# Performance work log

Hardware: AMD Instinct MI355X
Metric: run time of the kernel (lower is better)

Reference implementation:

```python
import jax, jax.numpy as jnp
import numpy as np

WIN = (8, 7, 7)
SHIFT = (4, 3, 3)
HEADS = 4
DIM = 128
VOL = WIN[0] * WIN[1] * WIN[2]  # 392


def _rel_index():
    coords = np.stack(np.meshgrid(np.arange(WIN[0]), np.arange(WIN[1]), np.arange(WIN[2]), indexing='ij'))
    cf = coords.reshape(3, -1)
    rel = (cf[:, :, None] - cf[:, None, :]).transpose(1, 2, 0).astype(np.int64)
    rel[..., 0] += WIN[0] - 1
    rel[..., 1] += WIN[1] - 1
    rel[..., 2] += WIN[2] - 1
    rel[..., 0] *= (2 * WIN[1] - 1) * (2 * WIN[2] - 1)
    rel[..., 1] *= 2 * WIN[2] - 1
    return rel.sum(-1)  # [VOL, VOL]


def _attn_mask(tp, hp, wp):
    m = np.zeros((tp, hp, wp))
    slices = [((0, -WIN[i]), (-WIN[i], -SHIFT[i]), (-SHIFT[i], None)) for i in range(3)]
    cnt = 0
    for d in slices[0]:
        for h in slices[1]:
            for w in slices[2]:
                m[d[0]:d[1], h[0]:h[1], w[0]:w[1]] = cnt
                cnt += 1
    m = m.reshape(tp // WIN[0], WIN[0], hp // WIN[1], WIN[1], wp // WIN[2], WIN[2])
    m = m.transpose(0, 2, 4, 1, 3, 5).reshape(-1, VOL)  # [nW, VOL]
    diff = m[:, None, :] - m[:, :, None]
    return np.where(diff != 0, -100.0, 0.0).astype(np.float32)  # [nW, VOL, VOL]


_REL_IDX = _rel_index()


def setup_inputs() -> dict:
    key = jax.random.key(0)
    ks = jax.random.split(key, 6)
    return {
        'x': jax.random.normal(ks[0], (2, 16, 56, 56, DIM), dtype=jnp.float32),
        'qkv_weight': jax.random.normal(ks[1], (3 * DIM, DIM), dtype=jnp.float32) * 0.02,
        'qkv_bias': jax.random.normal(ks[2], (3 * DIM,), dtype=jnp.float32) * 0.02,
        'proj_weight': jax.random.normal(ks[3], (DIM, DIM), dtype=jnp.float32) * 0.02,
        'proj_bias': jax.random.normal(ks[4], (DIM,), dtype=jnp.float32) * 0.02,
        'rel_bias_table': jax.random.normal(ks[5], ((2 * WIN[0] - 1) * (2 * WIN[1] - 1) * (2 * WIN[2] - 1), HEADS), dtype=jnp.float32) * 0.02,
    }


def reference(x, qkv_weight, qkv_bias, proj_weight, proj_bias, rel_bias_table):
    b, t, h, w, c = x.shape
    hd = c // HEADS
    nt, nh, nw = t // WIN[0], h // WIN[1], w // WIN[2]
    NW = nt * nh * nw

    # relative position bias: [1, HEADS, VOL, VOL]
    bias = rel_bias_table[jnp.asarray(_REL_IDX.flatten())]
    bias = bias.reshape(VOL, VOL, HEADS).transpose(2, 0, 1)[None]

    # cyclic shift
    xs = jnp.roll(x, shift=(-SHIFT[0], -SHIFT[1], -SHIFT[2]), axis=(1, 2, 3))

    # window partition -> [B*NW, VOL, C]
    xw = xs.reshape(b, nt, WIN[0], nh, WIN[1], nw, WIN[2], c)
    xw = xw.transpose(0, 1, 3, 5, 2, 4, 6, 7).reshape(b * NW, VOL, c)

    qkv = xw @ qkv_weight.T + qkv_bias
    qkv = qkv.reshape(b * NW, VOL, 3, HEADS, hd).transpose(2, 0, 3, 1, 4)
    q, k, v = qkv[0] * (hd ** -0.5), qkv[1], qkv[2]

    attn = jnp.einsum('nhqd,nhkd->nhqk', q, k) + bias
    mask = jnp.asarray(_attn_mask(t, h, w))  # [NW, VOL, VOL]
    attn = attn.reshape(b, NW, HEADS, VOL, VOL) + mask[None, :, None]
    attn = jax.nn.softmax(attn, axis=-1).reshape(b * NW, HEADS, VOL, VOL)

    out = jnp.einsum('nhqk,nhkd->nqhd', attn, v).reshape(b * NW, VOL, c)
    out = out @ proj_weight.T + proj_bias

    # window reverse
    out = out.reshape(b, nt, nh, nw, WIN[0], WIN[1], WIN[2], c)
    out = out.transpose(0, 1, 4, 2, 5, 3, 6, 7).reshape(b, t, h, w, c)
    out = jnp.roll(out, shift=SHIFT, axis=(1, 2, 3))
    return out
```

## Files before the change

### kernel.cpp

```cpp
#include <hip/hip_runtime.h>


#define DIMC   128
#define HEADS  4
#define HD     32
#define VOL    392
#define VPAD   416
#define TQ     400
#define TK     416
#define SCALE2 0.25503490443f
#define LOG2E  1.4426950408889634f
#define MASK2  144.26950408889634f

typedef __bf16 bf16;
typedef __attribute__((ext_vector_type(8))) __bf16 bf16x8;
typedef __attribute__((ext_vector_type(4))) __bf16 bf16x4;
typedef __attribute__((ext_vector_type(2))) __bf16 bf16x2;
typedef __attribute__((ext_vector_type(4))) float  f32x4;

#define OFF_VT  (392*32)
#define VTCOLS  424
#define LDS_ELEMS (392*32 + 32*VTCOLS)
#define AW_BYTES (256ull * VPAD * DIMC * 2ull)

static __device__ inline bf16x8 pack8(float4 a, float4 b) {
    bf16x8 r;
    r[0] = (bf16)a.x; r[1] = (bf16)a.y; r[2] = (bf16)a.z; r[3] = (bf16)a.w;
    r[4] = (bf16)b.x; r[5] = (bf16)b.y; r[6] = (bf16)b.z; r[7] = (bf16)b.w;
    return r;
}
static __device__ inline bf16x8 zero8() {
    bf16x8 z;
#pragma unroll
    for (int i = 0; i < 8; ++i) z[i] = (bf16)0.0f;
    return z;
}
static __device__ inline int swz4(int row) { return ((row >> 1) ^ (row >> 3)) & 3; }

static __device__ inline unsigned pkbf(float a, float b) {
    bf16x2 t; t[0] = (bf16)a; t[1] = (bf16)b;
    return __builtin_bit_cast(unsigned, t);
}

#if defined(__has_builtin)
#if __has_builtin(__builtin_amdgcn_exp2f)
#define HAS_EXP2 1
#endif
#endif
static __device__ inline float exp2_hw(float x) {
#ifdef HAS_EXP2
    return __builtin_amdgcn_exp2f(x);
#else
    float r; asm volatile("v_exp_f32 %0, %1\n\ts_nop 0" : "=v"(r) : "v"(x)); return r;
#endif
}

__global__ __launch_bounds__(256) void gen_table(const float* __restrict__ btab,
                                                 bf16* __restrict__ tbl) {
    const int idx = blockIdx.x * 256 + threadIdx.x;
    const int total = 8 * HEADS * TQ * (TK / 4);
    if (idx >= total) return;
    const int k4  = (idx % (TK / 4)) * 4;
    const int q   = (idx / (TK / 4)) % TQ;
    const int h   = (idx / ((TK / 4) * TQ)) & 3;
    const int pat = idx / ((TK / 4) * TQ * HEADS);
    const int tb = (pat >> 2) & 1, hb = (pat >> 1) & 1, wb = pat & 1;

    int qt = 0, qh = 0, qw = 0, lq = 0;
    if (q < VOL) {
        qt = q / 49; const int qr = q - qt * 49; qh = qr / 7; qw = qr - qh * 7;
        lq = (tb ? (qt < 4 ? 1 : 2) : 0) * 9 + (hb ? (qh < 4 ? 1 : 2) : 0) * 3 +
             (wb ? (qw < 4 ? 1 : 2) : 0);
    }
    bf16x4 out;
#pragma unroll
    for (int j = 0; j < 4; ++j) {
        const int k = k4 + j;
        float v;
        if (k >= VOL)      v = -30000.0f;
        else if (q >= VOL) v = 0.0f;
        else {
            const int kt = k / 49; const int kr = k - kt * 49;
            const int kh = kr / 7; const int kw = kr - kh * 7;
            const int rel = ((qt - kt + 7) * 13 + (qh - kh + 6)) * 13 + (qw - kw + 6);
            v = btab[rel * HEADS + h] * LOG2E;
            const int lk = (tb ? (kt < 4 ? 1 : 2) : 0) * 9 +
                           (hb ? (kh < 4 ? 1 : 2) : 0) * 3 +
                           (wb ? (kw < 4 ? 1 : 2) : 0);
            if (lq != lk) v -= MASK2;
        }
        out[j] = (bf16)v;
    }
    *(bf16x4*)&tbl[((size_t)(pat * HEADS + h) * TQ + q) * TK + k4] = out;
}

#define NJ 7

__global__ __attribute__((amdgpu_flat_work_group_size(256, 256),
                          amdgpu_waves_per_eu(2, 4)))
void swin_attn(
    const float* __restrict__ x, const float* __restrict__ wqkv,
    const float* __restrict__ bqkv, const bf16* __restrict__ tbl,
    bf16* __restrict__ aw)
{
    __shared__ __align__(16) bf16 lds[LDS_ELEMS];

    const int bid  = blockIdx.x;
    const int xcd  = bid & 7;
    const int tt   = bid >> 3;
    const int win  = xcd * 32 + (tt >> 2);
    const int head = tt & 3;
    const int b    = win >> 7;
    const int wrem = win & 127;
    const int it   = wrem >> 6;
    const int ih   = (wrem >> 3) & 7;
    const int iw   = wrem & 7;
    const int pat  = ((it == 1) ? 4 : 0) | ((ih == 7) ? 2 : 0) | ((iw == 7) ? 1 : 0);

    const int tid  = threadIdx.x;
    const int lane = tid & 63;
    const int wv   = tid >> 6;
    const int l16  = lane & 15;
    const int lg   = lane >> 4;

    {
        const int rowp = tid >> 3, colp = VPAD + (tid & 7);
        lds[OFF_VT + rowp * VTCOLS + colp] = (bf16)0.0f;
    }

    const bf16* tblh = tbl + (size_t)(pat * HEADS + head) * (TQ * TK);

    bf16x8 wfr[6][4];
    float  bcol[4];
#pragma unroll
    for (int o = 0; o < 6; ++o) {
        const int g = o >> 1, h2 = o & 1;
        const int wrow = g * DIMC + head * HD + h2 * 16 + l16;
        const float* wp = wqkv + (size_t)wrow * DIMC + 8 * lg;
#pragma unroll
        for (int ks = 0; ks < 4; ++ks)
            wfr[o][ks] = pack8(*(const float4*)(wp + ks * 32),
                               *(const float4*)(wp + ks * 32 + 4));
        if (o < 4) bcol[o] = bqkv[wrow];
    }
    float bvr[2][4];
#pragma unroll
    for (int h2 = 0; h2 < 2; ++h2)
#pragma unroll
        for (int r = 0; r < 4; ++r)
            bvr[h2][r] = bqkv[2 * DIMC + head * HD + h2 * 16 + lg * 4 + r];

    bf16x8 qf[NJ];
#pragma unroll
    for (int j = 0; j < NJ; ++j) qf[j] = zero8();

#pragma unroll
    for (int j = 0; j < NJ; ++j) {
        const int mt = wv + 4 * j;
        if (mt < 26) {
            const int tv = mt * 16 + l16;
            bf16x8 af[4];
            if (tv < VOL) {
                const int lt = tv / 49, rr = tv - lt * 49;
                const int lh = rr / 7,  lw = rr - lh * 7;
                const int t0 = (it * 8 + lt + 4) & 15;
                int h0 = ih * 7 + lh + 3; if (h0 >= 56) h0 -= 56;
                int w0 = iw * 7 + lw + 3; if (w0 >= 56) w0 -= 56;
                const float* xp = x + (size_t)(((b * 16 + t0) * 56 + h0) * 56 + w0) * DIMC + 8 * lg;
#pragma unroll
                for (int ks = 0; ks < 4; ++ks)
                    af[ks] = pack8(*(const float4*)(xp + ks * 32),
                                   *(const float4*)(xp + ks * 32 + 4));
            } else {
#pragma unroll
                for (int ks = 0; ks < 4; ++ks) af[ks] = zero8();
            }
#pragma unroll
            for (int o = 0; o < 2; ++o) {
                f32x4 acc = {0.f, 0.f, 0.f, 0.f};
#pragma unroll
                for (int ks = 0; ks < 4; ++ks)
                    acc = __builtin_amdgcn_mfma_f32_16x16x32_bf16(af[ks], wfr[o][ks], acc, 0, 0, 0);
                const int cb = (o & 1) * 16 + l16;
#pragma unroll
                for (int r = 0; r < 4; ++r) {
                    const int row = mt * 16 + lg * 4 + r;
                    if (row < VOL)
                        lds[row * 32 + (cb ^ (swz4(row) << 3))] = (bf16)((acc[r] + bcol[o]) * SCALE2);
                }
            }
            if (mt < 25) {
                const int qr = (tv < VOL) ? tv : (VOL - 1);
                qf[j] = *(const bf16x8*)&lds[qr * 32 + ((lg * 8) ^ (swz4(qr) << 3))];
            }
#pragma unroll
            for (int o = 2; o < 4; ++o) {
                f32x4 acc = {0.f, 0.f, 0.f, 0.f};
#pragma unroll
                for (int ks = 0; ks < 4; ++ks)
                    acc = __builtin_amdgcn_mfma_f32_16x16x32_bf16(af[ks], wfr[o][ks], acc, 0, 0, 0);
                const int cb = (o & 1) * 16 + l16;
#pragma unroll
                for (int r = 0; r < 4; ++r) {
                    const int row = mt * 16 + lg * 4 + r;
                    if (row < VOL)
                        lds[row * 32 + (cb ^ (swz4(row) << 3))] = (bf16)(acc[r] + bcol[o]);
                }
            }
#pragma unroll
            for (int h2 = 0; h2 < 2; ++h2) {
                f32x4 acc = {0.f, 0.f, 0.f, 0.f};
#pragma unroll
                for (int ks = 0; ks < 4; ++ks)
                    acc = __builtin_amdgcn_mfma_f32_16x16x32_bf16(wfr[4 + h2][ks], af[ks], acc, 0, 0, 0);
#pragma unroll
                for (int r = 0; r < 4; ++r) {
                    const int n = h2 * 16 + lg * 4 + r;
                    lds[OFF_VT + n * VTCOLS + (tv ^ (swz4(n) << 3))] = (bf16)(acc[r] + bvr[h2][r]);
                }
            }
        }
    }
    __syncthreads();

    {
        const int c = l16 & 3, d = l16 >> 2;
        const int rowA  = c + 8 * d;
        const int swzA  = (c >> 1) ^ d;
        const int swzB  = (2 + (c >> 1)) ^ d;
        const int kbA   = rowA * 32       + ((lg * 8) ^ (swzA << 3));
        const int kbB   = (rowA + 4) * 32 + ((lg * 8) ^ (swzB << 3));
        const int vb0   = OFF_VT + l16 * VTCOLS        + ((lg * 8) ^ (swz4(l16) << 3));
        const int vb1   = OFF_VT + (16 + l16) * VTCOLS + ((lg * 8) ^ (swz4(16 + l16) << 3));

        int    tbOff[NJ];
        f32x4  o0[NJ], o1[NJ];
        float  sum[NJ];
#pragma unroll
        for (int j = 0; j < NJ; ++j) {
            const int qtok = (wv + 4 * j) * 16 + l16;
            const int qc   = (qtok < TQ) ? qtok : (TQ - 1);
            tbOff[j] = (qc * TK + 8 * lg) * 2;
            o0[j] = f32x4{0.f, 0.f, 0.f, 0.f};
            o1[j] = f32x4{0.f, 0.f, 0.f, 0.f};
            sum[j] = 0.f;
        }

        uint4 bufA[NJ], bufB[NJ];
        bf16x8 kA0, kB0, v00, v10, kA1, kB1, v01, v11;

#define CH_PREB(CH, DST)                                                      \
        {                                                                     \
            const int chp_ = (CH) < 12 ? (CH) : 12;                           \
            _Pragma("unroll")                                                 \
            for (int j = 0; j < NJ; ++j)                                      \
                DST[j] = *(const uint4*)((const char*)tblh + tbOff[j] + chp_ * 64); \
        }
#define CH_PREF(CH, KA, KB, V0, V1)                                           \
        {                                                                     \
            const int chf_ = (CH) < 12 ? (CH) : 12;                           \
            KA = *(const bf16x8*)&lds[kbA + chf_ * 1024];                     \
            KB = *(const bf16x8*)&lds[kbB + chf_ * 1024];                     \
            V0 = *(const bf16x8*)&lds[vb0 + chf_ * 32];                       \
            V1 = *(const bf16x8*)&lds[vb1 + chf_ * 32];                       \
        }
#define CH_BODY(CUR, KA, KB, V0, V1)                                          \
        {                                                                     \
            _Pragma("unroll")                                                 \
            for (int j = 0; j < NJ; ++j) {                                    \
                if (wv + 4 * j < 25) {                                        \
                    const uint4 bu = CUR[j];                                  \
                    f32x4 cA, cB;                                             \
                    cA[0] = __builtin_bit_cast(float, bu.x << 16);            \
                    cA[1] = __builtin_bit_cast(float, bu.x & 0xffff0000u);    \
                    cA[2] = __builtin_bit_cast(float, bu.y << 16);            \
                    cA[3] = __builtin_bit_cast(float, bu.y & 0xffff0000u);    \
                    cB[0] = __builtin_bit_cast(float, bu.z << 16);            \
                    cB[1] = __builtin_bit_cast(float, bu.z & 0xffff0000u);    \
                    cB[2] = __builtin_bit_cast(float, bu.w << 16);            \
                    cB[3] = __builtin_bit_cast(float, bu.w & 0xffff0000u);    \
                    const f32x4 sA = __builtin_amdgcn_mfma_f32_16x16x32_bf16(KA, qf[j], cA, 0, 0, 0); \
                    const f32x4 sB = __builtin_amdgcn_mfma_f32_16x16x32_bf16(KB, qf[j], cB, 0, 0, 0); \
                    float pA[4], pB[4];                                       \
                    _Pragma("unroll")                                         \
                    for (int r = 0; r < 4; ++r) {                             \
                        pA[r] = exp2_hw(sA[r]);                               \
                        pB[r] = exp2_hw(sB[r]);                               \
                        sum[j] += pA[r] + pB[r];                              \
                    }                                                         \
                    union { unsigned u[4]; bf16x8 v; } pw;                    \
                    pw.u[0] = pkbf(pA[0], pA[1]); pw.u[1] = pkbf(pA[2], pA[3]); \
                    pw.u[2] = pkbf(pB[0], pB[1]); pw.u[3] = pkbf(pB[2], pB[3]); \
                    o0[j] = __builtin_amdgcn_mfma_f32_16x16x32_bf16(V0, pw.v, o0[j], 0, 0, 0); \
                    o1[j] = __builtin_amdgcn_mfma_f32_16x16x32_bf16(V1, pw.v, o1[j], 0, 0, 0); \
                }                                                             \
            }                                                                 \
        }

        CH_PREB(0, bufA)
        CH_PREF(0, kA0, kB0, v00, v10)

#pragma unroll 1
        for (int chp = 0; chp < 12; chp += 2) {
            CH_PREF(chp + 1, kA1, kB1, v01, v11)
            CH_PREB(chp + 1, bufB)
            CH_BODY(bufA, kA0, kB0, v00, v10)
            CH_PREF(chp + 2, kA0, kB0, v00, v10)
            CH_PREB(chp + 2, bufA)
            CH_BODY(bufB, kA1, kB1, v01, v11)
        }
        CH_BODY(bufA, kA0, kB0, v00, v10)
#undef CH_BODY
#undef CH_PREB
#undef CH_PREF

#pragma unroll
        for (int j = 0; j < NJ; ++j) {
            const int mt   = wv + 4 * j;
            const int qtok = mt * 16 + l16;
            if (mt < 25) {
                float s = sum[j];
                s += __shfl_xor(s, 16);
                s += __shfl_xor(s, 32);
                const float inv = 1.0f / s;
                if (qtok < VOL) {
                    bf16x4 w0, w1;
#pragma unroll
                    for (int r = 0; r < 4; ++r) {
                        w0[r] = (bf16)(o0[j][r] * inv);
                        w1[r] = (bf16)(o1[j][r] * inv);
                    }
                    bf16* op = aw + ((size_t)win * VPAD + qtok) * DIMC + head * HD + lg * 4;
                    *(bf16x4*)op = w0;
                    *(bf16x4*)(op + 16) = w1;
                }
            }
        }
    }
}

__global__ __launch_bounds__(256, 2) void swin_proj(
    const bf16* __restrict__ aw, const float* __restrict__ wproj,
    const float* __restrict__ bproj, float* __restrict__ out)
{
    const int bid  = blockIdx.x;
    const int xcd  = bid & 7;
    const int rest = bid >> 3;
    const int win  = xcd * 32 + (rest & 31);
    const int half = rest >> 5;
    const int b    = win >> 7;
    const int wrem = win & 127;
    const int it   = wrem >> 6;
    const int ih   = (wrem >> 3) & 7;
    const int iw   = wrem & 7;

    const int tid  = threadIdx.x;
    const int lane = tid & 63;
    const int wid  = tid >> 6;
    const int l16  = lane & 15;
    const int lg   = lane >> 4;

    const int mt_end = half ? 25 : 13;
    for (int mt = 13 * half + wid; mt < mt_end; mt += 4) {
        bf16x8 af[4];
        const bf16* ap = aw + ((size_t)win * VPAD + mt * 16 + l16) * DIMC + 8 * lg;
#pragma unroll
        for (int ks = 0; ks < 4; ++ks) af[ks] = *(const bf16x8*)(ap + ks * 32);

        float* ob[4]; bool qok[4];
#pragma unroll
        for (int r = 0; r < 4; ++r) {
            int q = mt * 16 + lg * 4 + r;
            qok[r] = q < VOL; if (!qok[r]) q = 0;
            const int lt = q / 49, rr = q - lt * 49;
            const int lh = rr / 7, lw = rr - lh * 7;
            const int t0 = (it * 8 + lt + 4) & 15;
            int h0 = ih * 7 + lh + 3; if (h0 >= 56) h0 -= 56;
            int w0 = iw * 7 + lw + 3; if (w0 >= 56) w0 -= 56;
            ob[r] = out + (size_t)(((b * 16 + t0) * 56 + h0) * 56 + w0) * DIMC;
        }
#pragma unroll
        for (int nt = 0; nt < 8; ++nt) {
            f32x4 acc = {0.f, 0.f, 0.f, 0.f};
            const float* wp = wproj + (size_t)(nt * 16 + l16) * DIMC + 8 * lg;
#pragma unroll
            for (int ks = 0; ks < 4; ++ks) {
                float4 u0 = *(const float4*)(wp + ks * 32);
                float4 u1 = *(const float4*)(wp + ks * 32 + 4);
                acc = __builtin_amdgcn_mfma_f32_16x16x32_bf16(af[ks], pack8(u0, u1), acc, 0, 0, 0);
            }
            const float bv = bproj[nt * 16 + l16];
#pragma unroll
            for (int r = 0; r < 4; ++r)
                if (qok[r]) ob[r][nt * 16 + l16] = acc[r] + bv;
        }
    }
}

extern "C" void kernel_launch(void* const* d_in, const int* in_sizes, int n_in,
                              void* d_out, int out_size, void* d_ws, size_t ws_size,
                              hipStream_t stream) {
    const float* x     = (const float*)d_in[0];
    const float* wqkv  = (const float*)d_in[1];
    const float* bqkv  = (const float*)d_in[2];
    const float* wproj = (const float*)d_in[3];
    const float* bproj = (const float*)d_in[4];
    const float* btab  = (const float*)d_in[5];
    bf16*  aw  = (bf16*)d_ws;
    bf16*  tbl = (bf16*)((char*)d_ws + AW_BYTES);
    float* out = (float*)d_out;

    const int tbl_threads = 8 * HEADS * TQ * (TK / 4);
    gen_table<<<dim3((tbl_threads + 255) / 256), dim3(256), 0, stream>>>(btab, tbl);
    swin_attn<<<dim3(1024), dim3(256), 0, stream>>>(x, wqkv, bqkv, tbl, aw);
    swin_proj<<<dim3(512), dim3(256), 0, stream>>>(aw, wproj, bproj, out);
}
```

Before: 129.2 us.

## Compute softmax row sums with an MFMA against ones and drop LDS fragment prefetch

The softmax denominator is now accumulated by an extra MFMA that multiplies the bf16 probabilities by a ones vector. This replaces the per-lane scalar adds and the cross-lane shuffle reduction. The explicit double-buffered LDS prefetch of K/V fragments is removed in favour of loading them inline per chunk, and each chunk body is wrapped in s_setprio raise and lower. The aim is to cut VALU work and register pressure. The costs are one more MFMA per tile, less hiding of LDS latency, and a sum taken from bf16-rounded probabilities rather than fp32 values.

Measured after the change: 123.6 us. 1.04x faster.

```diff
diff --git a/kernel.cpp b/kernel.cpp
--- a/kernel.cpp
+++ b/kernel.cpp
@@ -33,6 +33,12 @@
     bf16x8 z;
 #pragma unroll
     for (int i = 0; i < 8; ++i) z[i] = (bf16)0.0f;
+    return z;
+}
+static __device__ inline bf16x8 ones8() {
+    bf16x8 z;
+#pragma unroll
+    for (int i = 0; i < 8; ++i) z[i] = (bf16)1.0f;
     return z;
 }
 static __device__ inline int swz4(int row) { return ((row >> 1) ^ (row >> 3)) & 3; }
@@ -232,22 +238,21 @@
         const int kbB   = (rowA + 4) * 32 + ((lg * 8) ^ (swzB << 3));
         const int vb0   = OFF_VT + l16 * VTCOLS        + ((lg * 8) ^ (swz4(l16) << 3));
         const int vb1   = OFF_VT + (16 + l16) * VTCOLS + ((lg * 8) ^ (swz4(16 + l16) << 3));
+        const bf16x8 onesf = ones8();
 
         int    tbOff[NJ];
-        f32x4  o0[NJ], o1[NJ];
-        float  sum[NJ];
+        f32x4  o0[NJ], o1[NJ], sumv[NJ];
 #pragma unroll
         for (int j = 0; j < NJ; ++j) {
             const int qtok = (wv + 4 * j) * 16 + l16;
             const int qc   = (qtok < TQ) ? qtok : (TQ - 1);
             tbOff[j] = (qc * TK + 8 * lg) * 2;
-            o0[j] = f32x4{0.f, 0.f, 0.f, 0.f};
-            o1[j] = f32x4{0.f, 0.f, 0.f, 0.f};
-            sum[j] = 0.f;
+            o0[j]   = f32x4{0.f, 0.f, 0.f, 0.f};
+            o1[j]   = f32x4{0.f, 0.f, 0.f, 0.f};
+            sumv[j] = f32x4{0.f, 0.f, 0.f, 0.f};
         }
 
         uint4 bufA[NJ], bufB[NJ];
-        bf16x8 kA0, kB0, v00, v10, kA1, kB1, v01, v11;
 
 #define CH_PREB(CH, DST)                                                      \
         {                                                                     \
@@ -256,16 +261,14 @@
             for (int j = 0; j < NJ; ++j)                                      \
                 DST[j] = *(const uint4*)((const char*)tblh + tbOff[j] + chp_ * 64); \
         }
-#define CH_PREF(CH, KA, KB, V0, V1)                                           \
+#define CH_BODY(CH, CUR)                                                      \
         {                                                                     \
-            const int chf_ = (CH) < 12 ? (CH) : 12;                           \
-            KA = *(const bf16x8*)&lds[kbA + chf_ * 1024];                     \
-            KB = *(const bf16x8*)&lds[kbB + chf_ * 1024];                     \
-            V0 = *(const bf16x8*)&lds[vb0 + chf_ * 32];                       \
-            V1 = *(const bf16x8*)&lds[vb1 + chf_ * 32];                       \
-        }
-#define CH_BODY(CUR, KA, KB, V0, V1)                                          \
-        {                                                                     \
+            const int ch = (CH);                                              \
+            const bf16x8 kfA = *(const bf16x8*)&lds[kbA + ch * 1024];         \
+            const bf16x8 kfB = *(const bf16x8*)&lds[kbB + ch * 1024];         \
+            const bf16x8 v0  = *(const bf16x8*)&lds[vb0 + ch * 32];           \
+            const bf16x8 v1  = *(const bf16x8*)&lds[vb1 + ch * 32];           \
+            __builtin_amdgcn_s_setprio(1);                                    \
             _Pragma("unroll")                                                 \
             for (int j = 0; j < NJ; ++j) {                                    \
                 if (wv + 4 * j < 25) {                                        \
@@ -279,50 +282,40 @@
                     cB[1] = __builtin_bit_cast(float, bu.z & 0xffff0000u);    \
                     cB[2] = __builtin_bit_cast(float, bu.w << 16);            \
                     cB[3] = __builtin_bit_cast(float, bu.w & 0xffff0000u);    \
-                    const f32x4 sA = __builtin_amdgcn_mfma_f32_16x16x32_bf16(KA, qf[j], cA, 0, 0, 0); \
-                    const f32x4 sB = __builtin_amdgcn_mfma_f32_16x16x32_bf16(KB, qf[j], cB, 0, 0, 0); \
-                    float pA[4], pB[4];                                       \
-                    _Pragma("unroll")                                         \
-                    for (int r = 0; r < 4; ++r) {                             \
-                        pA[r] = exp2_hw(sA[r]);                               \
-                        pB[r] = exp2_hw(sB[r]);                               \
-                        sum[j] += pA[r] + pB[r];                              \
-                    }                                                         \
+                    const f32x4 sA = __builtin_amdgcn_mfma_f32_16x16x32_bf16(kfA, qf[j], cA, 0, 0, 0); \
+                    const f32x4 sB = __builtin_amdgcn_mfma_f32_16x16x32_bf16(kfB, qf[j], cB, 0, 0, 0); \
                     union { unsigned u[4]; bf16x8 v; } pw;                    \
-                    pw.u[0] = pkbf(pA[0], pA[1]); pw.u[1] = pkbf(pA[2], pA[3]); \
-                    pw.u[2] = pkbf(pB[0], pB[1]); pw.u[3] = pkbf(pB[2], pB[3]); \
-                    o0[j] = __builtin_amdgcn_mfma_f32_16x16x32_bf16(V0, pw.v, o0[j], 0, 0, 0); \
-                    o1[j] = __builtin_amdgcn_mfma_f32_16x16x32_bf16(V1, pw.v, o1[j], 0, 0, 0); \
+                    pw.u[0] = pkbf(exp2_hw(sA[0]), exp2_hw(sA[1]));           \
+                    pw.u[1] = pkbf(exp2_hw(sA[2]), exp2_hw(sA[3]));           \
+                    pw.u[2] = pkbf(exp2_hw(sB[0]), exp2_hw(sB[1]));           \
+                    pw.u[3] = pkbf(exp2_hw(sB[2]), exp2_hw(sB[3]));           \
+                    o0[j]   = __builtin_amdgcn_mfma_f32_16x16x32_bf16(v0, pw.v, o0[j], 0, 0, 0);   \
+                    o1[j]   = __builtin_amdgcn_mfma_f32_16x16x32_bf16(v1, pw.v, o1[j], 0, 0, 0);   \
+                    sumv[j] = __builtin_amdgcn_mfma_f32_16x16x32_bf16(onesf, pw.v, sumv[j], 0, 0, 0); \
                 }                                                             \
             }                                                                 \
+            __builtin_amdgcn_s_setprio(0);                                    \
         }
 
         CH_PREB(0, bufA)
-        CH_PREF(0, kA0, kB0, v00, v10)
 
 #pragma unroll 1
         for (int chp = 0; chp < 12; chp += 2) {
-            CH_PREF(chp + 1, kA1, kB1, v01, v11)
             CH_PREB(chp + 1, bufB)
-            CH_BODY(bufA, kA0, kB0, v00, v10)
-            CH_PREF(chp + 2, kA0, kB0, v00, v10)
+            CH_BODY(chp, bufA)
             CH_PREB(chp + 2, bufA)
-            CH_BODY(bufB, kA1, kB1, v01, v11)
-        }
-        CH_BODY(bufA, kA0, kB0, v00, v10)
+            CH_BODY(chp + 1, bufB)
+        }
+        CH_BODY(12, bufA)
 #undef CH_BODY
 #undef CH_PREB
-#undef CH_PREF
 
 #pragma unroll
         for (int j = 0; j < NJ; ++j) {
             const int mt   = wv + 4 * j;
             const int qtok = mt * 16 + l16;
             if (mt < 25) {
-                float s = sum[j];
-                s += __shfl_xor(s, 16);
-                s += __shfl_xor(s, 32);
-                const float inv = 1.0f / s;
+                const float inv = 1.0f / sumv[j][0];
                 if (qtok < VOL) {
                     bf16x4 w0, w1;
 #pragma unroll
```
